# Kernel tuning notes

Hardware: AMD Instinct MI355X
Metric: run time of the kernel (lower is better)

The kernel has to match this reference:

```python
import jax, jax.numpy as jnp
import numpy as np

D_MODEL = 1024
NUM_HEADS = 16
D_K = D_MODEL // NUM_HEADS


def setup_inputs() -> dict:
    key = jax.random.key(0)
    ks = jax.random.split(key, 9)
    s = 1.0 / np.sqrt(D_MODEL)
    x = jax.random.normal(ks[0], (1, 4096, D_MODEL), dtype=jnp.float32)
    Wq = jax.random.uniform(ks[1], (D_MODEL, D_MODEL), jnp.float32, -s, s)
    bq = jax.random.uniform(ks[2], (D_MODEL,), jnp.float32, -s, s)
    Wk = jax.random.uniform(ks[3], (D_MODEL, D_MODEL), jnp.float32, -s, s)
    bk = jax.random.uniform(ks[4], (D_MODEL,), jnp.float32, -s, s)
    Wv = jax.random.uniform(ks[5], (D_MODEL, D_MODEL), jnp.float32, -s, s)
    bv = jax.random.uniform(ks[6], (D_MODEL,), jnp.float32, -s, s)
    Wo = jax.random.uniform(ks[7], (D_MODEL, D_MODEL), jnp.float32, -s, s)
    bo = jax.random.uniform(ks[8], (D_MODEL,), jnp.float32, -s, s)
    return {"x": x, "Wq": Wq, "bq": bq, "Wk": Wk, "bk": bk,
            "Wv": Wv, "bv": bv, "Wo": Wo, "bo": bo}


def reference(x, Wq, bq, Wk, bk, Wv, bv, Wo, bo):
    B, S, _ = x.shape
    scale = jnp.sqrt(jnp.asarray(D_K, dtype=x.dtype))
    # projections (torch Linear: y = x @ W.T + b)
    q = (x @ Wq.T + bq).reshape(B, S, NUM_HEADS, D_K).transpose(0, 2, 1, 3)
    k = (x @ Wk.T + bk).reshape(B, S, NUM_HEADS, D_K).transpose(0, 2, 1, 3)
    v = (x @ Wv.T + bv).reshape(B, S, NUM_HEADS, D_K).transpose(0, 2, 1, 3)
    # [B, H, S, S] naive scores, causal mask, softmax
    scores = jnp.einsum('bhqd,bhkd->bhqk', q, k) / scale
    causal = jnp.tril(jnp.ones((S, S), dtype=bool))
    scores = jnp.where(causal, scores, jnp.asarray(-jnp.inf, dtype=scores.dtype))
    probs = jax.nn.softmax(scores, axis=-1)
    out = jnp.einsum('bhqk,bhkd->bhqd', probs, v)
    out = out.transpose(0, 2, 1, 3).reshape(B, S, D_MODEL)
    return out @ Wo.T + bo
```

## Files before the change

### kernel.cpp

```cpp
#include <hip/hip_runtime.h>
#include <math.h>

#define SEQ 4096
#define DMODEL 1024
#define NH 16
#define DK 64
#define LDP 72

typedef __bf16    bf16x8 __attribute__((ext_vector_type(8)));
typedef float     f32x4  __attribute__((ext_vector_type(4)));
typedef __fp16    fp16x2 __attribute__((ext_vector_type(2)));
typedef _Float16  h16x2  __attribute__((ext_vector_type(2)));
typedef _Float16  h16x4  __attribute__((ext_vector_type(4)));
typedef _Float16  h16x8  __attribute__((ext_vector_type(8)));

#define GLOAD_LDS16(g, l) __builtin_amdgcn_global_load_lds(                     \
    (const __attribute__((address_space(1))) unsigned int*)(g),                 \
    (__attribute__((address_space(3))) unsigned int*)(l), 16, 0, 0)

__device__ __forceinline__ h16x2 cvt_pk_h16(float a, float b) {
    fp16x2 r = __builtin_amdgcn_cvt_pkrtz(a, b);
    return __builtin_bit_cast(h16x2, r);
}

#define EXP2R(x) __builtin_amdgcn_exp2f(x)

__global__ __launch_bounds__(256)
void cvt_all(const float* __restrict__ x, const float* __restrict__ Wq,
             const float* __restrict__ Wk, const float* __restrict__ Wv,
             const float* __restrict__ Wo, __bf16* __restrict__ dst)
{
    const size_t M1 = 1u << 20;
    const size_t e = ((size_t)blockIdx.x * 256 + threadIdx.x) * 8;
    const float* src; size_t off;
    if      (e < 4*M1) { src = x;  off = e;        }
    else if (e < 5*M1) { src = Wq; off = e - 4*M1; }
    else if (e < 6*M1) { src = Wk; off = e - 5*M1; }
    else if (e < 7*M1) { src = Wv; off = e - 6*M1; }
    else               { src = Wo; off = e - 7*M1; }
    const float4 f0 = *reinterpret_cast<const float4*>(&src[off]);
    const float4 f1 = *reinterpret_cast<const float4*>(&src[off + 4]);
    bf16x8 pk;
    pk[0]=(__bf16)f0.x; pk[1]=(__bf16)f0.y; pk[2]=(__bf16)f0.z; pk[3]=(__bf16)f0.w;
    pk[4]=(__bf16)f1.x; pk[5]=(__bf16)f1.y; pk[6]=(__bf16)f1.z; pk[7]=(__bf16)f1.w;
    *reinterpret_cast<bf16x8*>(&dst[e]) = pk;
}

__device__ __forceinline__ void gemm_core128(const __bf16* __restrict__ A,
                                             const __bf16* __restrict__ W,
                                             int m0, int n0, int t,
                                             __bf16* AsF, __bf16* BsF,
                                             f32x4 acc[4][4])
{
    const int w = t >> 6, lane = t & 63, l15 = lane & 15, quad = lane >> 4;
    const int wm = (w & 1) * 64, wn = (w >> 1) * 64;
    const int lr = lane >> 3, lc = lane & 7;
    for (int k0 = 0; k0 < DMODEL; k0 += 64) {
        __syncthreads();
        #pragma unroll
        for (int p = 0; p < 4; ++p) {
            const int n = w*4 + p;
            const int r = n*8 + lr;
            const int cl = lc ^ (r & 7);
            GLOAD_LDS16(&A[(size_t)(m0 + r) * DMODEL + k0 + cl*8], &AsF[n*512]);
            GLOAD_LDS16(&W[(size_t)(n0 + r) * DMODEL + k0 + cl*8], &BsF[n*512]);
        }
        __syncthreads();
        #pragma unroll
        for (int kb = 0; kb < 2; ++kb) {
            const int phys = ((kb*4 + quad) ^ (l15 & 7)) * 8;
            bf16x8 af[4], bfr[4];
            #pragma unroll
            for (int i = 0; i < 4; ++i) {
                af[i]  = *reinterpret_cast<const bf16x8*>(&AsF[(wm + i*16 + l15)*64 + phys]);
                bfr[i] = *reinterpret_cast<const bf16x8*>(&BsF[(wn + i*16 + l15)*64 + phys]);
            }
            #pragma unroll
            for (int ms = 0; ms < 4; ++ms)
                #pragma unroll
                for (int ns = 0; ns < 4; ++ns)
                    acc[ms][ns] = __builtin_amdgcn_mfma_f32_16x16x32_bf16(af[ms], bfr[ns], acc[ms][ns], 0, 0, 0);
        }
    }
}

__global__ __launch_bounds__(256, 3)
void gemm_qkv(const __bf16* __restrict__ xb, const __bf16* __restrict__ Wcat,
              const float* __restrict__ bq, const float* __restrict__ bk,
              const float* __restrict__ bv,
              _Float16* __restrict__ Qh, _Float16* __restrict__ Kh, _Float16* __restrict__ Vth)
{
    __shared__ __bf16 SM[4*64*LDP];
    __bf16* AsF = SM;
    __bf16* BsF = SM + 8192;
    const int t = threadIdx.x;
    const int n0g = blockIdx.x * 128;
    const int m0  = blockIdx.y * 128;
    const int which = n0g >> 10;
    const int n_in  = n0g & 1023;

    f32x4 acc[4][4] = {};
    gemm_core128(xb, Wcat, m0, n0g, t, AsF, BsF, acc);

    const int w = t >> 6, lane = t & 63, l15 = lane & 15, quad = lane >> 4;
    const int wm = (w & 1) * 64, wn = (w >> 1) * 64;
    const float* bias = (which == 0) ? bq : (which == 1) ? bk : bv;
    float br[4];
    #pragma unroll
    for (int ns = 0; ns < 4; ++ns) br[ns] = bias[n_in + wn + ns*16 + l15];

    if (which == 2) {
        #pragma unroll
        for (int ms = 0; ms < 4; ++ms)
            #pragma unroll
            for (int ns = 0; ns < 4; ++ns) {
                h16x4 pk;
                #pragma unroll
                for (int rg = 0; rg < 4; ++rg) pk[rg] = (_Float16)(acc[ms][ns][rg] + br[ns]);
                *reinterpret_cast<h16x4*>(
                    &Vth[(size_t)(n_in + wn + ns*16 + l15) * SEQ + m0 + wm + ms*16 + quad*4]) = pk;
            }
    } else {
        const float s = (which == 0) ? 0.1803368787f : 1.0f;
        _Float16* C = (which == 0) ? Qh : Kh;
        __syncthreads();
        _Float16* tile = (_Float16*)SM + w * 64 * LDP;
        #pragma unroll
        for (int ms = 0; ms < 4; ++ms)
            #pragma unroll
            for (int ns = 0; ns < 4; ++ns)
                #pragma unroll
                for (int rg = 0; rg < 4; ++rg)
                    tile[(ms*16 + quad*4 + rg) * LDP + ns*16 + l15] =
                        (_Float16)((acc[ms][ns][rg] + br[ns]) * s);
        asm volatile("s_waitcnt lgkmcnt(0)" ::: "memory");
        const int er = lane >> 3, ec = (lane & 7) * 8;
        #pragma unroll
        for (int p = 0; p < 8; ++p) {
            const h16x8 v = *reinterpret_cast<const h16x8*>(&tile[(er + p*8) * LDP + ec]);
            *reinterpret_cast<h16x8*>(
                &C[(size_t)(m0 + wm + er + p*8) * DMODEL + n_in + wn + ec]) = v;
        }
    }
}

__device__ __forceinline__ void gemm_core64(const __bf16* __restrict__ A,
                                            const __bf16* __restrict__ W,
                                            int m0, int n0, int t,
                                            __bf16* AsF, __bf16* BsF,
                                            f32x4 acc[2][4])
{
    const int w = t >> 6, lane = t & 63, l15 = lane & 15, quad = lane >> 4;
    const int lr = lane >> 3, lc = lane & 7;
    for (int k0 = 0; k0 < DMODEL; k0 += 64) {
        __syncthreads();
        #pragma unroll
        for (int p = 0; p < 4; ++p) {
            const int n = w*4 + p;
            const int r = n*8 + lr;
            const int cl = lc ^ (r & 7);
            GLOAD_LDS16(&A[(size_t)(m0 + r) * DMODEL + k0 + cl*8], &AsF[n*512]);
        }
        #pragma unroll
        for (int p = 0; p < 2; ++p) {
            const int n = w*2 + p;
            const int r = n*8 + lr;
            const int cl = lc ^ (r & 7);
            GLOAD_LDS16(&W[(size_t)(n0 + r) * DMODEL + k0 + cl*8], &BsF[n*512]);
        }
        __syncthreads();
        #pragma unroll
        for (int kb = 0; kb < 2; ++kb) {
            const int phys = ((kb*4 + quad) ^ (l15 & 7)) * 8;
            bf16x8 af0 = *reinterpret_cast<const bf16x8*>(&AsF[(w*32 + l15)*64 + phys]);
            bf16x8 af1 = *reinterpret_cast<const bf16x8*>(&AsF[(w*32 + 16 + l15)*64 + phys]);
            #pragma unroll
            for (int ns = 0; ns < 4; ++ns) {
                const bf16x8 bfr = *reinterpret_cast<const bf16x8*>(&BsF[(ns*16 + l15)*64 + phys]);
                acc[0][ns] = __builtin_amdgcn_mfma_f32_16x16x32_bf16(af0, bfr, acc[0][ns], 0, 0, 0);
                acc[1][ns] = __builtin_amdgcn_mfma_f32_16x16x32_bf16(af1, bfr, acc[1][ns], 0, 0, 0);
            }
        }
    }
}

__global__ __launch_bounds__(256, 4)
void gemm_out(const __bf16* __restrict__ Ob, const __bf16* __restrict__ Wob,
              const float* __restrict__ bo, float* __restrict__ out)
{
    __shared__ __bf16 AsF[128*64];
    __shared__ __bf16 BsF[64*64];
    const int t = threadIdx.x;
    const int n0 = blockIdx.x * 64;
    const int m0 = blockIdx.y * 128;

    f32x4 acc[2][4] = {};
    gemm_core64(Ob, Wob, m0, n0, t, AsF, BsF, acc);

    const int lane = t & 63, l15 = lane & 15, quad = lane >> 4, w = t >> 6;
    float br[4];
    #pragma unroll
    for (int ns = 0; ns < 4; ++ns) br[ns] = bo[n0 + ns*16 + l15];
    #pragma unroll
    for (int ms = 0; ms < 2; ++ms)
        #pragma unroll
        for (int ns = 0; ns < 4; ++ns)
            #pragma unroll
            for (int rg = 0; rg < 4; ++rg)
                out[(size_t)(m0 + w*32 + ms*16 + quad*4 + rg) * DMODEL + n0 + ns*16 + l15] =
                    acc[ms][ns][rg] + br[ns];
}

__global__ __launch_bounds__(256, 3)
void attn_mfma(const _Float16* __restrict__ Q, const _Float16* __restrict__ K,
               const _Float16* __restrict__ Vt, __bf16* __restrict__ O,
               float* __restrict__ part, float* __restrict__ lpart)
{
    __shared__ _Float16 KsF[2][64*64];
    __shared__ _Float16 VsF[2][64*64];

    const int t = threadIdx.x;
    const int w = t >> 6;
    const int lane = t & 63, l15 = lane & 15, quad = lane >> 4;
    const int lr = lane >> 3, lc = lane & 7;
    const int h = blockIdx.y;
    const int u = blockIdx.x;
    int qt, g;
    if      (u < 16) { qt = 16 + u; g = 0; }
    else if (u < 32) { qt = u;      g = 1; }
    else             { qt = 47 - u; g = 0; }
    const int tstart = g * 32;
    const int tlast  = 2*qt + 1;
    const int tend   = (tlast < tstart + 31) ? tlast : (tstart + 31);
    const int s0 = qt*128 + w*16;
    const int s1 = s0 + 64;

    h16x8 bq8[2][2];
    #pragma unroll
    for (int kb = 0; kb < 2; ++kb) {
        bq8[0][kb] = *reinterpret_cast<const h16x8*>(
            &Q[(size_t)(s0 + l15) * DMODEL + h*DK + kb*32 + quad*8]);
        bq8[1][kb] = *reinterpret_cast<const h16x8*>(
            &Q[(size_t)(s1 + l15) * DMODEL + h*DK + kb*32 + quad*8]);
    }

    const int cl = lc ^ lr;
    const int rA = (w*2 + 0)*8 + lr, rB = (w*2 + 1)*8 + lr;
    const int dA = (w*2 + 0)*512,   dB = (w*2 + 1)*512;
    const _Float16* kpA = &K [(size_t)(tstart*64 + rA) * DMODEL + h*DK + cl*8];
    const _Float16* kpB = &K [(size_t)(tstart*64 + rB) * DMODEL + h*DK + cl*8];
    const _Float16* vpA = &Vt[(size_t)(h*DK + rA) * SEQ + tstart*64 + cl*8];
    const _Float16* vpB = &Vt[(size_t)(h*DK + rB) * SEQ + tstart*64 + cl*8];

#define STAGE_KV(bi) do {                                     \
        GLOAD_LDS16(kpA, &KsF[bi][dA]);                       \
        GLOAD_LDS16(kpB, &KsF[bi][dB]);                       \
        GLOAD_LDS16(vpA, &VsF[bi][dA]);                       \
        GLOAD_LDS16(vpB, &VsF[bi][dB]);                       \
        kpA += (size_t)64*DMODEL; kpB += (size_t)64*DMODEL;   \
        vpA += 64; vpB += 64; } while (0)

    f32x4 acc[2][4] = {};
    f32x4 accl[2] = {};
    const h16x4 vone = {(_Float16)1.f, (_Float16)1.f, (_Float16)1.f, (_Float16)1.f};

    STAGE_KV(0);
    __syncthreads();

    int pbuf = 0;
    for (int tk = tstart; tk <= tend; ++tk, pbuf ^= 1) {
        if (tk < tend) STAGE_KV(pbuf ^ 1);

        const int j0 = tk * 64;
        const bool act0 = (j0 <= s0 + 15);
        const bool msk0 = (j0 + 63 > s0);
        const bool msk1 = (j0 + 63 > s1);
        const int rel0 = s0 - j0 + l15;
        const int rel1 = s1 - j0 + l15;

        h16x4 ap[2][4];
        #pragma unroll
        for (int st = 0; st < 4; ++st) {
            const h16x8 ak0 = *reinterpret_cast<const h16x8*>(
                &KsF[pbuf][(st*16 + l15)*64 + ((quad ^ (l15 & 7)))*8]);
            const h16x8 ak1 = *reinterpret_cast<const h16x8*>(
                &KsF[pbuf][(st*16 + l15)*64 + (((4 + quad) ^ (l15 & 7)))*8]);
            {
                f32x4 cc = {0.f, 0.f, 0.f, 0.f};
                cc = __builtin_amdgcn_mfma_f32_16x16x32_f16(ak0, bq8[1][0], cc, 0, 0, 0);
                cc = __builtin_amdgcn_mfma_f32_16x16x32_f16(ak1, bq8[1][1], cc, 0, 0, 0);
                float pv[4];
                if (msk1) {
                    #pragma unroll
                    for (int rg = 0; rg < 4; ++rg) {
                        const float e = EXP2R(cc[rg]);
                        pv[rg] = (st*16 + quad*4 + rg > rel1) ? 0.f : e;
                    }
                } else {
                    #pragma unroll
                    for (int rg = 0; rg < 4; ++rg) pv[rg] = EXP2R(cc[rg]);
                }
                const h16x2 lo = cvt_pk_h16(pv[0], pv[1]);
                const h16x2 hi = cvt_pk_h16(pv[2], pv[3]);
                ap[1][st] = (h16x4){lo[0], lo[1], hi[0], hi[1]};
                accl[1] = __builtin_amdgcn_mfma_f32_16x16x16f16(ap[1][st], vone, accl[1], 0, 0, 0);
            }
            if (act0) {
                f32x4 cc = {0.f, 0.f, 0.f, 0.f};
                cc = __builtin_amdgcn_mfma_f32_16x16x32_f16(ak0, bq8[0][0], cc, 0, 0, 0);
                cc = __builtin_amdgcn_mfma_f32_16x16x32_f16(ak1, bq8[0][1], cc, 0, 0, 0);
                float pv[4];
                if (msk0) {
                    #pragma unroll
                    for (int rg = 0; rg < 4; ++rg) {
                        const float e = EXP2R(cc[rg]);
                        pv[rg] = (st*16 + quad*4 + rg > rel0) ? 0.f : e;
                    }
                } else {
                    #pragma unroll
                    for (int rg = 0; rg < 4; ++rg) pv[rg] = EXP2R(cc[rg]);
                }
                const h16x2 lo = cvt_pk_h16(pv[0], pv[1]);
                const h16x2 hi = cvt_pk_h16(pv[2], pv[3]);
                ap[0][st] = (h16x4){lo[0], lo[1], hi[0], hi[1]};
                accl[0] = __builtin_amdgcn_mfma_f32_16x16x16f16(ap[0][st], vone, accl[0], 0, 0, 0);
            }
        }

        #pragma unroll
        for (int ds_ = 0; ds_ < 4; ++ds_) {
            #pragma unroll
            for (int st = 0; st < 4; ++st) {
                const h16x4 bv = *reinterpret_cast<const h16x4*>(
                    &VsF[pbuf][(ds_*16 + l15)*64 +
                               (((st*2 + (quad >> 1)) ^ (l15 & 7)))*8 + (quad & 1)*4]);
                acc[1][ds_] = __builtin_amdgcn_mfma_f32_16x16x16f16(ap[1][st], bv, acc[1][ds_], 0, 0, 0);
                if (act0)
                    acc[0][ds_] = __builtin_amdgcn_mfma_f32_16x16x16f16(ap[0][st], bv, acc[0][ds_], 0, 0, 0);
            }
        }
        __syncthreads();
    }
#undef STAGE_KV

    if (qt < 16) {
        #pragma unroll
        for (int s = 0; s < 2; ++s) {
            const int base = s ? s1 : s0;
            #pragma unroll
            for (int rg = 0; rg < 4; ++rg) {
                const float inv = 1.0f / accl[s][rg];
                const size_t row = (size_t)(base + quad*4 + rg) * DMODEL + h * DK;
                #pragma unroll
                for (int ds_ = 0; ds_ < 4; ++ds_)
                    O[row + ds_*16 + l15] = (__bf16)(acc[s][ds_][rg] * inv);
            }
        }
    } else {
        const int unit = (h*16 + (qt - 16))*2 + g;
        const size_t pbase = (size_t)unit * 8192;
        #pragma unroll
        for (int s = 0; s < 2; ++s) {
            #pragma unroll
            for (int rg = 0; rg < 4; ++rg) {
                const int lrow = s*64 + w*16 + quad*4 + rg;
                #pragma unroll
                for (int ds_ = 0; ds_ < 4; ++ds_)
                    part[pbase + lrow*64 + ds_*16 + l15] = acc[s][ds_][rg];
            }
            if (l15 == 0) {
                #pragma unroll
                for (int rg = 0; rg < 4; ++rg)
                    lpart[unit*128 + s*64 + w*16 + quad*4 + rg] = accl[s][rg];
            }
        }
    }
}

__global__ __launch_bounds__(256)
void attn_combine(const float* __restrict__ part, const float* __restrict__ lpart,
                  __bf16* __restrict__ O)
{
    const int t = threadIdx.x;
    const int qtp = blockIdx.x;
    const int h = blockIdx.y;
    const int u0 = (h*16 + qtp)*2;
    const size_t b0 = (size_t)u0 * 8192;
    const size_t b1 = b0 + 8192;
    const int r  = t >> 1;
    const int d0 = (t & 1) * 32;

    const float l = lpart[u0*128 + r] + lpart[(u0 + 1)*128 + r];
    const float inv = 1.0f / l;
    const size_t grow = (size_t)((16 + qtp)*128 + r) * DMODEL + h*64 + d0;
    #pragma unroll
    for (int i = 0; i < 4; ++i) {
        bf16x8 pk;
        #pragma unroll
        for (int j = 0; j < 2; ++j) {
            const float4 p0 = *reinterpret_cast<const float4*>(&part[b0 + r*64 + d0 + i*8 + j*4]);
            const float4 p1 = *reinterpret_cast<const float4*>(&part[b1 + r*64 + d0 + i*8 + j*4]);
            pk[j*4+0] = (__bf16)((p0.x + p1.x) * inv);
            pk[j*4+1] = (__bf16)((p0.y + p1.y) * inv);
            pk[j*4+2] = (__bf16)((p0.z + p1.z) * inv);
            pk[j*4+3] = (__bf16)((p0.w + p1.w) * inv);
        }
        *reinterpret_cast<bf16x8*>(&O[grow + i*8]) = pk;
    }
}

extern "C" void kernel_launch(void* const* d_in, const int* in_sizes, int n_in,
                              void* d_out, int out_size, void* d_ws, size_t ws_size,
                              hipStream_t stream) {
    const float* x  = (const float*)d_in[0];
    const float* Wq = (const float*)d_in[1];
    const float* bq = (const float*)d_in[2];
    const float* Wk = (const float*)d_in[3];
    const float* bk = (const float*)d_in[4];
    const float* Wv = (const float*)d_in[5];
    const float* bv = (const float*)d_in[6];
    const float* Wo = (const float*)d_in[7];
    const float* bo = (const float*)d_in[8];
    float* out = (float*)d_out;

    const size_t M1 = 1u << 20;
    __bf16* base = (__bf16*)d_ws;
    __bf16*    xb   = base;
    __bf16*    Wcat = base + 4*M1;
    __bf16*    Wob  = base + 7*M1;
    _Float16*  Qh   = (_Float16*)(base + 8*M1);
    _Float16*  Kh   = (_Float16*)(base + 12*M1);
    _Float16*  Vth  = (_Float16*)(base + 16*M1);
    __bf16*    Ob   = base + 20*M1;
    float*     lpart = (float*)(base + 24*M1);
    float*     part  = out;

    cvt_all<<<4096, 256, 0, stream>>>(x, Wq, Wk, Wv, Wo, base);
    gemm_qkv<<<dim3(24, 32), 256, 0, stream>>>(xb, Wcat, bq, bk, bv, Qh, Kh, Vth);
    attn_mfma<<<dim3(48, NH), 256, 0, stream>>>(Qh, Kh, Vth, Ob, part, lpart);
    attn_combine<<<dim3(16, NH), 256, 0, stream>>>(part, lpart, Ob);
    gemm_out<<<dim3(16, 32), 256, 0, stream>>>(Ob, Wob, bo, out);
}
```

Measured before the change: 220.0 us.

## Rebalance causal attention with table-driven KV splits and fp16 partials

Replaces the fixed two-way KV split of the upper query tiles with lookup tables that assign 80 work units per head, splitting query tiles 8-31 into 2-4 KV chunks so per-block work is more uniform. Partial accumulators are stored as fp16 instead of fp32, halving partial-buffer traffic, and are spread across the output buffer and the now-dead x/W staging buffers. Occupancy hint is raised from 3 to 5 blocks per CU. The combine kernel now sums a variable number of chunks and adds precision loss from fp16 partials and more launch units.

```diff
diff --git a/kernel.cpp b/kernel.cpp
--- a/kernel.cpp
+++ b/kernel.cpp
@@ -24,6 +24,31 @@
 }
 
 #define EXP2R(x) __builtin_amdgcn_exp2f(x)
+
+__device__ const unsigned char UQT[80] = {
+     0, 1, 2, 3, 8, 8, 4, 9,  9,10,10,16,16,30,15,15,
+    31,30,29,14,21,21,20,13, 23,23,23,22, 7,30,22,12,
+    31,30,29,14,27,27,26,13, 22,26,25,24,19,11,11, 5,
+    31,29,28,28,27,20,26, 6, 26,25,25,18,19,17,17,16,
+    31,29,28,28,27,20,19,21, 24,25,24,18,12,17,18,24 };
+__device__ const unsigned char UTS[80] = {
+     0, 0, 0, 0, 0, 9, 0, 0, 10, 0,11,12,23,32, 0,16,
+     0, 0,30, 0, 0,15,28, 0,  0,16,32, 0, 0,47,31,13,
+    16,16,45,15, 0,42, 0,14, 16,41,26,13,14, 0,12, 0,
+    32, 0, 0,30,14, 0,14, 0, 28, 0,39, 0,27, 0,24, 0,
+    48,15,15,44,28,14, 0,30, 26,13, 0,13, 0,12,26,38 };
+__device__ const unsigned char UTE[80] = {
+     1, 3, 5, 7, 8,17, 9, 9, 19,10,21,22,33,46,15,31,
+    15,15,44,14,14,29,41,13, 15,31,47,15,15,61,45,25,
+    31,31,59,29,13,55,13,27, 30,53,38,25,26,11,23,11,
+    47,14,14,43,27,13,27,13, 40,12,51,12,39,11,35,11,
+    63,29,29,57,41,27,13,43, 37,25,12,25,12,23,37,49 };
+__device__ const signed char UPS[80] = {
+    -1,-1,-1,-1, 0, 1,-1, 2,  3, 4, 5,17,18,66,14,15,
+    68,64,62,12,31,32,30,10, 37,38,39,34,-1,67,36, 9,
+    69,65,63,13,52,55,48,11, 35,51,46,41,26, 6, 7,-1,
+    70,60,56,58,53,28,49,-1, 50,44,47,22,27,19,21,16,
+    71,61,57,59,54,29,25,33, 42,45,40,23, 8,20,24,43 };
 
 __global__ __launch_bounds__(256)
 void cvt_all(const float* __restrict__ x, const float* __restrict__ Wq,
@@ -211,10 +236,11 @@
                     acc[ms][ns][rg] + br[ns];
 }
 
-__global__ __launch_bounds__(256, 3)
+__global__ __launch_bounds__(256, 5)
 void attn_mfma(const _Float16* __restrict__ Q, const _Float16* __restrict__ K,
                const _Float16* __restrict__ Vt, __bf16* __restrict__ O,
-               float* __restrict__ part, float* __restrict__ lpart)
+               _Float16* __restrict__ partA, _Float16* __restrict__ partB,
+               float* __restrict__ lpart)
 {
     __shared__ _Float16 KsF[2][64*64];
     __shared__ _Float16 VsF[2][64*64];
@@ -225,13 +251,10 @@
     const int lr = lane >> 3, lc = lane & 7;
     const int h = blockIdx.y;
     const int u = blockIdx.x;
-    int qt, g;
-    if      (u < 16) { qt = 16 + u; g = 0; }
-    else if (u < 32) { qt = u;      g = 1; }
-    else             { qt = 47 - u; g = 0; }
-    const int tstart = g * 32;
-    const int tlast  = 2*qt + 1;
-    const int tend   = (tlast < tstart + 31) ? tlast : (tstart + 31);
+    const int qt     = UQT[u];
+    const int tstart = UTS[u];
+    const int tend   = UTE[u];
+    const int psl    = UPS[u];
     const int s0 = qt*128 + w*16;
     const int s1 = s0 + 64;
 
@@ -343,7 +366,7 @@
     }
 #undef STAGE_KV
 
-    if (qt < 16) {
+    if (psl < 0) {
         #pragma unroll
         for (int s = 0; s < 2; ++s) {
             const int base = s ? s1 : s0;
@@ -357,8 +380,9 @@
             }
         }
     } else {
-        const int unit = (h*16 + (qt - 16))*2 + g;
-        const size_t pbase = (size_t)unit * 8192;
+        const int slot = h*72 + psl;
+        _Float16* p = (slot < 1024) ? partA + (size_t)slot * 8192
+                                    : partB + (size_t)(slot - 1024) * 8192;
         #pragma unroll
         for (int s = 0; s < 2; ++s) {
             #pragma unroll
@@ -366,45 +390,47 @@
                 const int lrow = s*64 + w*16 + quad*4 + rg;
                 #pragma unroll
                 for (int ds_ = 0; ds_ < 4; ++ds_)
-                    part[pbase + lrow*64 + ds_*16 + l15] = acc[s][ds_][rg];
-            }
-            if (l15 == 0) {
-                #pragma unroll
-                for (int rg = 0; rg < 4; ++rg)
-                    lpart[unit*128 + s*64 + w*16 + quad*4 + rg] = accl[s][rg];
+                    p[lrow*64 + ds_*16 + l15] = (_Float16)acc[s][ds_][rg];
+                if (l15 == 0) lpart[(size_t)slot*128 + lrow] = accl[s][rg];
             }
         }
     }
 }
 
 __global__ __launch_bounds__(256)
-void attn_combine(const float* __restrict__ part, const float* __restrict__ lpart,
-                  __bf16* __restrict__ O)
+void attn_combine(const _Float16* __restrict__ partA, const _Float16* __restrict__ partB,
+                  const float* __restrict__ lpart, __bf16* __restrict__ O)
 {
     const int t = threadIdx.x;
-    const int qtp = blockIdx.x;
-    const int h = blockIdx.y;
-    const int u0 = (h*16 + qtp)*2;
-    const size_t b0 = (size_t)u0 * 8192;
-    const size_t b1 = b0 + 8192;
+    const int qt = 8 + blockIdx.x;
+    const int h  = blockIdx.y;
+    const int nc = (qt < 16) ? 2 : (qt < 24) ? 3 : 4;
+    const int pl = (qt < 16) ? (qt - 8)*2 : (qt < 24) ? 16 + (qt - 16)*3 : 40 + (qt - 24)*4;
+    const int sbase = h*72 + pl;
     const int r  = t >> 1;
     const int d0 = (t & 1) * 32;
 
-    const float l = lpart[u0*128 + r] + lpart[(u0 + 1)*128 + r];
+    float a[4][8] = {};
+    float l = 0.f;
+    for (int c = 0; c < nc; ++c) {
+        const int sl = sbase + c;
+        const _Float16* pc = (sl < 1024) ? partA + (size_t)sl * 8192
+                                         : partB + (size_t)(sl - 1024) * 8192;
+        l += lpart[(size_t)sl*128 + r];
+        #pragma unroll
+        for (int i = 0; i < 4; ++i) {
+            const h16x8 v = *reinterpret_cast<const h16x8*>(&pc[r*64 + d0 + i*8]);
+            #pragma unroll
+            for (int j = 0; j < 8; ++j) a[i][j] += (float)v[j];
+        }
+    }
     const float inv = 1.0f / l;
-    const size_t grow = (size_t)((16 + qtp)*128 + r) * DMODEL + h*64 + d0;
+    const size_t grow = (size_t)(qt*128 + r) * DMODEL + h*64 + d0;
     #pragma unroll
     for (int i = 0; i < 4; ++i) {
         bf16x8 pk;
         #pragma unroll
-        for (int j = 0; j < 2; ++j) {
-            const float4 p0 = *reinterpret_cast<const float4*>(&part[b0 + r*64 + d0 + i*8 + j*4]);
-            const float4 p1 = *reinterpret_cast<const float4*>(&part[b1 + r*64 + d0 + i*8 + j*4]);
-            pk[j*4+0] = (__bf16)((p0.x + p1.x) * inv);
-            pk[j*4+1] = (__bf16)((p0.y + p1.y) * inv);
-            pk[j*4+2] = (__bf16)((p0.z + p1.z) * inv);
-            pk[j*4+3] = (__bf16)((p0.w + p1.w) * inv);
-        }
+        for (int j = 0; j < 8; ++j) pk[j] = (__bf16)(a[i][j] * inv);
         *reinterpret_cast<bf16x8*>(&O[grow + i*8]) = pk;
     }
 }
@@ -432,12 +458,13 @@
     _Float16*  Kh   = (_Float16*)(base + 12*M1);
     _Float16*  Vth  = (_Float16*)(base + 16*M1);
     __bf16*    Ob   = base + 20*M1;
-    float*     lpart = (float*)(base + 24*M1);
-    float*     part  = out;
+    _Float16*  partA = (_Float16*)out;
+    _Float16*  partB = (_Float16*)xb;
+    float*     lpart = (float*)Wcat;
 
     cvt_all<<<4096, 256, 0, stream>>>(x, Wq, Wk, Wv, Wo, base);
     gemm_qkv<<<dim3(24, 32), 256, 0, stream>>>(xb, Wcat, bq, bk, bv, Qh, Kh, Vth);
-    attn_mfma<<<dim3(48, NH), 256, 0, stream>>>(Qh, Kh, Vth, Ob, part, lpart);
-    attn_combine<<<dim3(16, NH), 256, 0, stream>>>(part, lpart, Ob);
+    attn_mfma<<<dim3(80, NH), 256, 0, stream>>>(Qh, Kh, Vth, Ob, partA, partB, lpart);
+    attn_combine<<<dim3(24, NH), 256, 0, stream>>>(partA, partB, lpart, Ob);
     gemm_out<<<dim3(16, 32), 256, 0, stream>>>(Ob, Wob, bo, out);
 }
```

After: 277.0 us. +25.9%, slower.
